# Performance work log

Hardware: AMD Instinct MI355X
Metric: run time of the kernel (lower is better)

Reference implementation:

```python
import jax, jax.numpy as jnp
import numpy as np

K_TAPS = 4

def setup_inputs() -> dict:
    key = jax.random.key(0)
    ks = jax.random.split(key, 7)
    B, T, E, N, F, H, K = 4, 64, 1, 512, 32, 64, K_TAPS
    stdv = 1.0 / np.sqrt(F * K)
    x  = jax.random.normal(ks[0], (B, T, F, N), jnp.float32)
    z0 = jax.random.normal(ks[1], (B, H, N), jnp.float32)
    # scale GSO so repeated S-products stay bounded
    S  = jax.random.normal(ks[2], (B, T, E, N, N), jnp.float32) / np.sqrt(N)
    aW = jax.random.uniform(ks[3], (H, E, K, F), jnp.float32, -stdv, stdv)
    bW = jax.random.uniform(ks[4], (H, E, K, H), jnp.float32, -stdv, stdv)
    xBias = jax.random.uniform(ks[5], (H, 1), jnp.float32, -stdv, stdv)
    zBias = jax.random.uniform(ks[6], (H, 1), jnp.float32, -stdv, stdv)
    return {"x": x, "z0": z0, "S": S, "aW": aW, "bW": bW,
            "xBias": xBias, "zBias": zBias}

def _lsigf_db(h, S, x, b):
    # h: (F_out,E,K,G), S: (B,T,E,N,N), x: (B,T,G,N)
    B, T, G, N = x.shape
    E = S.shape[2]
    K = h.shape[2]
    xk = jnp.broadcast_to(x[:, :, None], (B, T, E, G, N))
    zs = [xk]
    for _ in range(1, K):
        # delay one step, then shift with current-time GSO: x(t-k) S(t-k+1)...S(t)
        xk = jnp.concatenate([jnp.zeros_like(xk[:, :1]), xk[:, :-1]], axis=1)
        xk = jnp.einsum('btegm,btemn->btegn', xk, S)
        zs.append(xk)
    z = jnp.stack(zs, axis=2)                      # (B,T,K,E,G,N)
    y = jnp.einsum('fekg,btkegn->btfn', h, z)      # (B,T,F_out,N)
    if b is not None:
        y = y + b
    return y

def reference(x, z0, S, aW, bW, xBias, zBias):
    B, T, F, N = x.shape
    H, E, K, _ = bW.shape
    sigma = jnp.tanh
    Ax = _lsigf_db(aW, S, x, xBias)                # (B,T,H,N)
    # delayed hidden-state stack, zero padded to K taps; tap 0 holds z0
    Sz0 = jnp.zeros((B, K, E, H, N), x.dtype).at[:, 0].set(
        jnp.broadcast_to(z0[:, None], (B, E, H, N)))
    Bz0 = jnp.einsum('hekg,bkegn->bhn', bW, Sz0) + zBias
    zt0 = sigma(Ax[:, 0] + Bz0)

    def step(carry, inp):
        zt, Sz = carry                             # zt:(B,H,N) Sz:(B,K,E,H,N)
        Axt, St = inp                              # Axt:(B,H,N) St:(B,E,N,N)
        tail = jnp.einsum('bkehm,bemn->bkehn', Sz[:, :K - 1], St)
        head = jnp.broadcast_to(zt[:, None, None], (B, 1, E, H, N))
        Sz = jnp.concatenate([head, tail], axis=1)
        Bzt = jnp.einsum('hekg,bkegn->bhn', bW, Sz) + zBias
        zt = sigma(Axt + Bzt)
        return (zt, Sz), zt

    Ax_rest = jnp.moveaxis(Ax[:, 1:], 1, 0)        # (T-1,B,H,N)
    S_rest = jnp.moveaxis(S[:, 1:], 1, 0)          # (T-1,B,E,N,N)
    _, z_rest = jax.lax.scan(step, (zt0, Sz0), (Ax_rest, S_rest))
    z = jnp.concatenate([zt0[:, None], jnp.moveaxis(z_rest, 0, 1)], axis=1)
    return z                                       # (B,T,H,N)
```

## Files before the change

### kernel.cpp

```cpp
#include <hip/hip_runtime.h>
#include <math.h>

#define B_  4
#define T_  64
#define F_  32
#define N_  512
#define H_  64

#define CN     32
#define NCB    (N_/CN)
#define AROWS  288
#define JW     384
#define NWAVES 9
#define NTHR   (NWAVES*64)

typedef __attribute__((ext_vector_type(8))) short short8;
typedef __attribute__((ext_vector_type(4))) float float4_;
typedef unsigned short u16;
typedef unsigned int   u32;

__device__ __host__ inline u16 f2bf(float x) {
    union { float f; u32 u; } v; v.f = x;
    u32 r = v.u + 0x7fff + ((v.u >> 16) & 1);
    return (u16)(r >> 16);
}
__device__ inline float bf2f(u16 h) {
    union { float f; u32 u; } v; v.u = ((u32)h) << 16;
    return v.f;
}

__global__ void init_wc(const float* __restrict__ aW, const float* __restrict__ bW,
                        const float* __restrict__ xB, const float* __restrict__ zB,
                        u16* __restrict__ Wch, u16* __restrict__ Wcl,
                        float* __restrict__ bsum) {
    int idx = blockIdx.x * blockDim.x + threadIdx.x;
    if (idx < H_ * JW) {
        int h = idx / JW, j = idx % JW;
        float w;
        if (j < 96)       w = aW[(h*4 + (j>>5) + 1)*F_ + (j&31)];
        else if (j < 288) { int jj = j - 96; w = bW[(h*4 + (jj>>6) + 1)*H_ + (jj&63)]; }
        else if (j < 320) w = aW[(h*4)*F_ + (j - 288)];
        else              w = bW[(h*4)*H_ + (j - 320)];
        u16 hi = f2bf(w);
        Wch[idx] = hi;
        Wcl[idx] = f2bf(w - bf2f(hi));
    }
    if (idx < H_) bsum[idx] = xB[idx] + zB[idx];
}

__global__ __launch_bounds__(NTHR) void step_kernel(
    const float* __restrict__ x, const float* __restrict__ z0,
    const float* __restrict__ S,
    const u16* __restrict__ Wch, const u16* __restrict__ Wcl,
    const float* __restrict__ bsum, float* __restrict__ out,
    const u16* __restrict__ Aph, const u16* __restrict__ Apl,
    u16* __restrict__ Anh, u16* __restrict__ Anl,
    int t)
{
    __shared__ __align__(16) u16 Slds[2][2][CN][40];
    __shared__ __align__(16) u32 Clds[2][CN][196];

    const int tid  = threadIdx.x;
    const int wave = tid >> 6;
    const int lane = tid & 63;
    const int c16  = lane & 15;
    const int g4   = lane >> 4;

    const int b  = blockIdx.x & 3;
    const int cb = blockIdx.x >> 2;
    const int n0 = cb * CN;

    const float* Sbt = S + (size_t)(b*T_ + t) * N_ * N_;

    if (tid < 512) {
        const int col = tid & 31;
        const int rb  = (tid >> 5) * 6;
        #pragma unroll
        for (int j = 0; j < 6; ++j) {
            int row = rb + j;
            float v; int arow;
            if (row < 32) {
                v = x[((size_t)(b*T_ + t)*F_ + row) * N_ + n0 + col];
                arow = row;
            } else {
                int hz = row - 32;
                v = (t == 0)
                    ? z0[((size_t)b*H_ + hz) * N_ + n0 + col]
                    : out[((size_t)(b*T_ + (t-1))*H_ + hz) * N_ + n0 + col];
                arow = 96 + hz;
            }
            u16 hi = f2bf(v);
            u16 lo = f2bf(v - bf2f(hi));
            ((u16*)&Clds[0][col][0])[288 + row] = hi;
            ((u16*)&Clds[1][col][0])[288 + row] = lo;
            size_t ai = ((size_t)b*AROWS + arow) * N_ + n0 + col;
            Anh[ai] = hi; Anl[ai] = lo;
        }
    }

    if (t == 0) {
        for (int i = tid; i < CN*144; i += NTHR) {
            int n = i / 144, rp = i % 144;
            Clds[0][n][rp] = 0; Clds[1][n][rp] = 0;
        }
        for (int i = tid; i < 192*(CN/2); i += NTHR) {
            int r = i / (CN/2), c2 = i % (CN/2);
            int arow = (r < 64) ? 32 + r : 96 + r;
            size_t ai = ((size_t)b*AROWS + arow) * N_ + n0;
            ((u32*)(Anh + ai))[c2] = 0;
            ((u32*)(Anl + ai))[c2] = 0;
        }
    } else {
        const int r0 = wave * 32;
        const u16* Ah0 = Aph + ((size_t)b*AROWS + r0 + c16) * N_;
        const u16* Al0 = Apl + ((size_t)b*AROWS + r0 + c16) * N_;

        auto stage = [&](int ks, int buf) {
            if (tid < 512) {
                int col = tid & 31;
                int rbase = tid >> 5;
                #pragma unroll
                for (int hh = 0; hh < 2; ++hh) {
                    int row = rbase + 16*hh;
                    float v = Sbt[(size_t)(ks*32 + row) * N_ + n0 + col];
                    u16 hi = f2bf(v);
                    u16 lo = f2bf(v - bf2f(hi));
                    Slds[buf][0][col][row] = hi;
                    Slds[buf][1][col][row] = lo;
                }
            }
        };

        float4_ acc[2][2];
        #pragma unroll
        for (int i = 0; i < 2; ++i)
            #pragma unroll
            for (int j = 0; j < 2; ++j) acc[i][j] = (float4_){0.f,0.f,0.f,0.f};

        stage(0, 0);
        short8 ah[2], al[2];
        #pragma unroll
        for (int rf = 0; rf < 2; ++rf) {
            ah[rf] = *(const short8*)(Ah0 + (size_t)rf*16*N_ + g4*8);
            al[rf] = *(const short8*)(Al0 + (size_t)rf*16*N_ + g4*8);
        }
        __syncthreads();

        for (int ks = 0; ks < 16; ++ks) {
            const int buf = ks & 1;
            if (ks < 15) stage(ks + 1, buf ^ 1);
            short8 ahn[2], aln[2];
            if (ks < 15) {
                #pragma unroll
                for (int rf = 0; rf < 2; ++rf) {
                    ahn[rf] = *(const short8*)(Ah0 + (size_t)rf*16*N_ + (ks+1)*32 + g4*8);
                    aln[rf] = *(const short8*)(Al0 + (size_t)rf*16*N_ + (ks+1)*32 + g4*8);
                }
            }
            short8 bh[2], bl[2];
            #pragma unroll
            for (int nf = 0; nf < 2; ++nf) {
                bh[nf] = *(const short8*)&Slds[buf][0][nf*16 + c16][g4*8];
                bl[nf] = *(const short8*)&Slds[buf][1][nf*16 + c16][g4*8];
            }
            #pragma unroll
            for (int rf = 0; rf < 2; ++rf)
                #pragma unroll
                for (int nf = 0; nf < 2; ++nf) {
                    acc[rf][nf] = __builtin_amdgcn_mfma_f32_16x16x32_bf16(ah[rf], bh[nf], acc[rf][nf], 0,0,0);
                    acc[rf][nf] = __builtin_amdgcn_mfma_f32_16x16x32_bf16(ah[rf], bl[nf], acc[rf][nf], 0,0,0);
                    acc[rf][nf] = __builtin_amdgcn_mfma_f32_16x16x32_bf16(al[rf], bh[nf], acc[rf][nf], 0,0,0);
                }
            if (ks < 15) {
                ah[0]=ahn[0]; ah[1]=ahn[1]; al[0]=aln[0]; al[1]=aln[1];
            }
            __syncthreads();
        }

        const int aoff = (wave < 2) ? 32 : (wave >= 3 && wave <= 6) ? 64 : -1;
        #pragma unroll
        for (int rf = 0; rf < 2; ++rf) {
            int crow = r0 + rf*16 + g4*4;
            int rp   = crow >> 1;
            #pragma unroll
            for (int nf = 0; nf < 2; ++nf) {
                int n = nf*16 + c16;
                float4_ a = acc[rf][nf];
                u16 h0=f2bf(a.x), h1=f2bf(a.y), h2=f2bf(a.z), h3=f2bf(a.w);
                u16 l0=f2bf(a.x - bf2f(h0)), l1=f2bf(a.y - bf2f(h1));
                u16 l2=f2bf(a.z - bf2f(h2)), l3=f2bf(a.w - bf2f(h3));
                Clds[0][n][rp]   = (u32)h0 | ((u32)h1 << 16);
                Clds[0][n][rp+1] = (u32)h2 | ((u32)h3 << 16);
                Clds[1][n][rp]   = (u32)l0 | ((u32)l1 << 16);
                Clds[1][n][rp+1] = (u32)l2 | ((u32)l3 << 16);
                if (aoff > 0) {
                    size_t base = ((size_t)b*AROWS + crow + aoff) * N_ + n0 + n;
                    Anh[base]        = h0; Anl[base]        = l0;
                    Anh[base +   N_] = h1; Anl[base +   N_] = l1;
                    Anh[base + 2*N_] = h2; Anl[base + 2*N_] = l2;
                    Anh[base + 3*N_] = h3; Anl[base + 3*N_] = l3;
                }
            }
        }
    }
    __syncthreads();

    if (wave < 8) {
        const int hf = wave >> 1;
        const int nf = wave & 1;
        float4_ a2 = (float4_){0.f,0.f,0.f,0.f};
        const u16* Wh0 = Wch + (size_t)(hf*16 + c16) * JW;
        const u16* Wl0 = Wcl + (size_t)(hf*16 + c16) * JW;
        const u16* Th = (const u16*)&Clds[0][nf*16 + c16][0];
        const u16* Tl = (const u16*)&Clds[1][nf*16 + c16][0];
        #pragma unroll 4
        for (int kf = 0; kf < 12; ++kf) {
            short8 wh = *(const short8*)(Wh0 + kf*32 + g4*8);
            short8 wl = *(const short8*)(Wl0 + kf*32 + g4*8);
            short8 th = *(const short8*)(Th + kf*32 + g4*8);
            short8 tl = *(const short8*)(Tl + kf*32 + g4*8);
            a2 = __builtin_amdgcn_mfma_f32_16x16x32_bf16(wh, th, a2, 0,0,0);
            a2 = __builtin_amdgcn_mfma_f32_16x16x32_bf16(wh, tl, a2, 0,0,0);
            a2 = __builtin_amdgcn_mfma_f32_16x16x32_bf16(wl, th, a2, 0,0,0);
        }
        const int h0r = hf*16 + g4*4;
        const float4 bsv = *(const float4*)(bsum + h0r);
        float zx = tanhf(a2.x + bsv.x);
        float zy = tanhf(a2.y + bsv.y);
        float zz = tanhf(a2.z + bsv.z);
        float zw = tanhf(a2.w + bsv.w);
        size_t ob = ((size_t)(b*T_ + t)*H_ + h0r) * N_ + n0 + nf*16 + c16;
        out[ob]        = zx;
        out[ob +   N_] = zy;
        out[ob + 2*N_] = zz;
        out[ob + 3*N_] = zw;
    }
}

extern "C" void kernel_launch(void* const* d_in, const int* in_sizes, int n_in,
                              void* d_out, int out_size, void* d_ws, size_t ws_size,
                              hipStream_t stream) {
    const float* x  = (const float*)d_in[0];
    const float* z0 = (const float*)d_in[1];
    const float* S  = (const float*)d_in[2];
    const float* aW = (const float*)d_in[3];
    const float* bW = (const float*)d_in[4];
    const float* xB = (const float*)d_in[5];
    const float* zB = (const float*)d_in[6];
    float* out = (float*)d_out;

    char* p = (char*)d_ws;
    u16*   Wch  = (u16*)p;   p += (size_t)H_*JW*2;
    u16*   Wcl  = (u16*)p;   p += (size_t)H_*JW*2;
    float* bsum = (float*)p; p += 256;
    const size_t asz = (size_t)B_*AROWS*N_*2;
    u16* Ah[2]; u16* Al[2];
    Ah[0] = (u16*)p; p += asz;
    Al[0] = (u16*)p; p += asz;
    Ah[1] = (u16*)p; p += asz;
    Al[1] = (u16*)p; p += asz;

    init_wc<<<96, 256, 0, stream>>>(aW, bW, xB, zB, Wch, Wcl, bsum);
    for (int t = 0; t < T_; ++t) {
        const int pb = t & 1, nb = pb ^ 1;
        step_kernel<<<B_*NCB, NTHR, 0, stream>>>(x, z0, S, Wch, Wcl, bsum, out,
                                                 Ah[pb], Al[pb], Ah[nb], Al[nb], t);
    }
}
```

Measured before the change: 2.463 ms.

## Fuse all timesteps into one persistent cooperative kernel with grid sync

Replaces the 64 per-timestep kernel launches with a single cooperative kernel that loops over time and uses grid.sync between steps. It halves the column stripe width so the grid has twice as many blocks, and caches the combined weight matrix in LDS once per block. It also prefetches the first S tile of the next timestep during the last k-step of the current one. This removes per-launch overhead and repeated global weight loads. In exchange it depends on cooperative launch residency, uses much more LDS per block, and gives each wave less MFMA work per step.

```diff
diff --git a/kernel.cpp b/kernel.cpp
--- a/kernel.cpp
+++ b/kernel.cpp
@@ -1,5 +1,8 @@
 #include <hip/hip_runtime.h>
+#include <hip/hip_cooperative_groups.h>
 #include <math.h>
+
+namespace cg = cooperative_groups;
 
 #define B_  4
 #define T_  64
@@ -7,12 +10,13 @@
 #define N_  512
 #define H_  64
 
-#define CN     32
-#define NCB    (N_/CN)
-#define AROWS  288
-#define JW     384
-#define NWAVES 9
-#define NTHR   (NWAVES*64)
+#define CN      16
+#define NSTRIPE (N_/CN)
+#define NBLK    (B_*NSTRIPE)
+#define AROWS   288
+#define JW      384
+#define NWAVES  9
+#define NTHR    (NWAVES*64)
 
 typedef __attribute__((ext_vector_type(8))) short short8;
 typedef __attribute__((ext_vector_type(4))) float float4_;
@@ -48,17 +52,19 @@
     if (idx < H_) bsum[idx] = xB[idx] + zB[idx];
 }
 
-__global__ __launch_bounds__(NTHR) void step_kernel(
+__global__ __launch_bounds__(NTHR, 1) void run_all(
     const float* __restrict__ x, const float* __restrict__ z0,
     const float* __restrict__ S,
     const u16* __restrict__ Wch, const u16* __restrict__ Wcl,
     const float* __restrict__ bsum, float* __restrict__ out,
-    const u16* __restrict__ Aph, const u16* __restrict__ Apl,
-    u16* __restrict__ Anh, u16* __restrict__ Anl,
-    int t)
+    u16* __restrict__ A0h, u16* __restrict__ A0l,
+    u16* __restrict__ A1h, u16* __restrict__ A1l)
 {
-    __shared__ __align__(16) u16 Slds[2][2][CN][40];
-    __shared__ __align__(16) u32 Clds[2][CN][196];
+    cg::grid_group grid = cg::this_grid();
+
+    __shared__ __align__(16) u16 Sld[2][2][CN][40];
+    __shared__ __align__(16) u32 Cl[2][CN][196];
+    __shared__ __align__(16) u16 Wl[2][H_][JW + 8];
 
     const int tid  = threadIdx.x;
     const int wave = tid >> 6;
@@ -66,135 +72,134 @@
     const int c16  = lane & 15;
     const int g4   = lane >> 4;
 
-    const int b  = blockIdx.x & 3;
-    const int cb = blockIdx.x >> 2;
-    const int n0 = cb * CN;
-
-    const float* Sbt = S + (size_t)(b*T_ + t) * N_ * N_;
-
-    if (tid < 512) {
-        const int col = tid & 31;
-        const int rb  = (tid >> 5) * 6;
-        #pragma unroll
-        for (int j = 0; j < 6; ++j) {
-            int row = rb + j;
-            float v; int arow;
-            if (row < 32) {
-                v = x[((size_t)(b*T_ + t)*F_ + row) * N_ + n0 + col];
-                arow = row;
-            } else {
-                int hz = row - 32;
-                v = (t == 0)
-                    ? z0[((size_t)b*H_ + hz) * N_ + n0 + col]
-                    : out[((size_t)(b*T_ + (t-1))*H_ + hz) * N_ + n0 + col];
-                arow = 96 + hz;
-            }
+    const int blk    = blockIdx.x;
+    const int b      = (blk & 7) >> 1;
+    const int stripe = ((blk >> 3) << 1) | (blk & 1);
+    const int n0     = stripe * CN;
+    const int r0     = wave * 32;
+
+    for (int i = tid; i < H_ * JW; i += NTHR) {
+        int h = i / JW, j = i % JW;
+        Wl[0][h][j] = Wch[i];
+        Wl[1][h][j] = Wcl[i];
+    }
+
+    auto stageS = [&](int tt, int ks, int buf) {
+        if (tid < 512) {
+            int n = tid & 15;
+            int k = tid >> 4;
+            const float* Sp = S + (size_t)(b*T_ + tt) * N_ * N_;
+            float v = Sp[(size_t)(ks*32 + k) * N_ + n0 + n];
             u16 hi = f2bf(v);
-            u16 lo = f2bf(v - bf2f(hi));
-            ((u16*)&Clds[0][col][0])[288 + row] = hi;
-            ((u16*)&Clds[1][col][0])[288 + row] = lo;
-            size_t ai = ((size_t)b*AROWS + arow) * N_ + n0 + col;
-            Anh[ai] = hi; Anl[ai] = lo;
-        }
-    }
-
-    if (t == 0) {
-        for (int i = tid; i < CN*144; i += NTHR) {
-            int n = i / 144, rp = i % 144;
-            Clds[0][n][rp] = 0; Clds[1][n][rp] = 0;
-        }
-        for (int i = tid; i < 192*(CN/2); i += NTHR) {
-            int r = i / (CN/2), c2 = i % (CN/2);
-            int arow = (r < 64) ? 32 + r : 96 + r;
-            size_t ai = ((size_t)b*AROWS + arow) * N_ + n0;
-            ((u32*)(Anh + ai))[c2] = 0;
-            ((u32*)(Anl + ai))[c2] = 0;
-        }
-    } else {
-        const int r0 = wave * 32;
-        const u16* Ah0 = Aph + ((size_t)b*AROWS + r0 + c16) * N_;
-        const u16* Al0 = Apl + ((size_t)b*AROWS + r0 + c16) * N_;
-
-        auto stage = [&](int ks, int buf) {
+            Sld[buf][0][n][k] = hi;
+            Sld[buf][1][n][k] = f2bf(v - bf2f(hi));
+        }
+    };
+
+    for (int t = 0; t < T_; ++t) {
+        const int par = t & 1;
+        const u16* Aph = par ? A1h : A0h;
+        const u16* Apl = par ? A1l : A0l;
+        u16* Anh = par ? A0h : A1h;
+        u16* Anl = par ? A0l : A1l;
+
+        if (tid < 512) {
+            const int col = tid & 15;
+            const int rb  = (tid >> 4) * 3;
+            #pragma unroll
+            for (int j = 0; j < 3; ++j) {
+                int row = rb + j;
+                float v; int arow;
+                if (row < 32) {
+                    v = x[((size_t)(b*T_ + t)*F_ + row) * N_ + n0 + col];
+                    arow = row;
+                } else {
+                    int hz = row - 32;
+                    v = (t == 0)
+                        ? z0[((size_t)b*H_ + hz) * N_ + n0 + col]
+                        : out[((size_t)(b*T_ + (t-1))*H_ + hz) * N_ + n0 + col];
+                    arow = 96 + hz;
+                }
+                u16 hi = f2bf(v);
+                u16 lo = f2bf(v - bf2f(hi));
+                ((u16*)&Cl[0][col][0])[288 + row] = hi;
+                ((u16*)&Cl[1][col][0])[288 + row] = lo;
+                size_t ai = ((size_t)b*AROWS + arow) * N_ + n0 + col;
+                Anh[ai] = hi; Anl[ai] = lo;
+            }
+        }
+
+        if (t == 0) {
+            for (int i = tid; i < CN*144; i += NTHR) {
+                int n = i / 144, rp = i % 144;
+                Cl[0][n][rp] = 0; Cl[1][n][rp] = 0;
+            }
             if (tid < 512) {
-                int col = tid & 31;
-                int rbase = tid >> 5;
+                int col = tid & 15, rb = (tid >> 4) * 6;
                 #pragma unroll
-                for (int hh = 0; hh < 2; ++hh) {
-                    int row = rbase + 16*hh;
-                    float v = Sbt[(size_t)(ks*32 + row) * N_ + n0 + col];
-                    u16 hi = f2bf(v);
-                    u16 lo = f2bf(v - bf2f(hi));
-                    Slds[buf][0][col][row] = hi;
-                    Slds[buf][1][col][row] = lo;
-                }
-            }
-        };
-
-        float4_ acc[2][2];
-        #pragma unroll
-        for (int i = 0; i < 2; ++i)
+                for (int j = 0; j < 6; ++j) {
+                    int r = rb + j;
+                    int arow = (r < 64) ? 32 + r : 96 + r;
+                    size_t ai = ((size_t)b*AROWS + arow) * N_ + n0 + col;
+                    Anh[ai] = 0; Anl[ai] = 0;
+                }
+            }
+            stageS(1, 0, 0);
+        } else {
+            const u16* Ah0 = Aph + ((size_t)b*AROWS + r0 + c16) * N_;
+            const u16* Al0 = Apl + ((size_t)b*AROWS + r0 + c16) * N_;
+
+            float4_ acc[2];
+            acc[0] = (float4_){0.f,0.f,0.f,0.f};
+            acc[1] = (float4_){0.f,0.f,0.f,0.f};
+
+            short8 ah[2], al[2];
             #pragma unroll
-            for (int j = 0; j < 2; ++j) acc[i][j] = (float4_){0.f,0.f,0.f,0.f};
-
-        stage(0, 0);
-        short8 ah[2], al[2];
-        #pragma unroll
-        for (int rf = 0; rf < 2; ++rf) {
-            ah[rf] = *(const short8*)(Ah0 + (size_t)rf*16*N_ + g4*8);
-            al[rf] = *(const short8*)(Al0 + (size_t)rf*16*N_ + g4*8);
-        }
-        __syncthreads();
-
-        for (int ks = 0; ks < 16; ++ks) {
-            const int buf = ks & 1;
-            if (ks < 15) stage(ks + 1, buf ^ 1);
-            short8 ahn[2], aln[2];
-            if (ks < 15) {
+            for (int rf = 0; rf < 2; ++rf) {
+                ah[rf] = *(const short8*)(Ah0 + (size_t)rf*16*N_ + g4*8);
+                al[rf] = *(const short8*)(Al0 + (size_t)rf*16*N_ + g4*8);
+            }
+            __syncthreads();
+
+            for (int ks = 0; ks < 16; ++ks) {
+                const int buf = ks & 1;
+                if (ks < 15)          stageS(t, ks + 1, buf ^ 1);
+                else if (t < T_ - 1)  stageS(t + 1, 0, 0);
+                short8 ahn[2], aln[2];
+                if (ks < 15) {
+                    #pragma unroll
+                    for (int rf = 0; rf < 2; ++rf) {
+                        ahn[rf] = *(const short8*)(Ah0 + (size_t)rf*16*N_ + (ks+1)*32 + g4*8);
+                        aln[rf] = *(const short8*)(Al0 + (size_t)rf*16*N_ + (ks+1)*32 + g4*8);
+                    }
+                }
+                short8 bh = *(const short8*)&Sld[buf][0][c16][g4*8];
+                short8 bl = *(const short8*)&Sld[buf][1][c16][g4*8];
                 #pragma unroll
                 for (int rf = 0; rf < 2; ++rf) {
-                    ahn[rf] = *(const short8*)(Ah0 + (size_t)rf*16*N_ + (ks+1)*32 + g4*8);
-                    aln[rf] = *(const short8*)(Al0 + (size_t)rf*16*N_ + (ks+1)*32 + g4*8);
-                }
-            }
-            short8 bh[2], bl[2];
+                    acc[rf] = __builtin_amdgcn_mfma_f32_16x16x32_bf16(ah[rf], bh, acc[rf], 0,0,0);
+                    acc[rf] = __builtin_amdgcn_mfma_f32_16x16x32_bf16(ah[rf], bl, acc[rf], 0,0,0);
+                    acc[rf] = __builtin_amdgcn_mfma_f32_16x16x32_bf16(al[rf], bh, acc[rf], 0,0,0);
+                }
+                if (ks < 15) { ah[0]=ahn[0]; ah[1]=ahn[1]; al[0]=aln[0]; al[1]=aln[1]; }
+                __syncthreads();
+            }
+
+            const int aoff = (wave < 2) ? 32 : (wave >= 3 && wave <= 6) ? 64 : -1;
             #pragma unroll
-            for (int nf = 0; nf < 2; ++nf) {
-                bh[nf] = *(const short8*)&Slds[buf][0][nf*16 + c16][g4*8];
-                bl[nf] = *(const short8*)&Slds[buf][1][nf*16 + c16][g4*8];
-            }
-            #pragma unroll
-            for (int rf = 0; rf < 2; ++rf)
-                #pragma unroll
-                for (int nf = 0; nf < 2; ++nf) {
-                    acc[rf][nf] = __builtin_amdgcn_mfma_f32_16x16x32_bf16(ah[rf], bh[nf], acc[rf][nf], 0,0,0);
-                    acc[rf][nf] = __builtin_amdgcn_mfma_f32_16x16x32_bf16(ah[rf], bl[nf], acc[rf][nf], 0,0,0);
-                    acc[rf][nf] = __builtin_amdgcn_mfma_f32_16x16x32_bf16(al[rf], bh[nf], acc[rf][nf], 0,0,0);
-                }
-            if (ks < 15) {
-                ah[0]=ahn[0]; ah[1]=ahn[1]; al[0]=aln[0]; al[1]=aln[1];
-            }
-            __syncthreads();
-        }
-
-        const int aoff = (wave < 2) ? 32 : (wave >= 3 && wave <= 6) ? 64 : -1;
-        #pragma unroll
-        for (int rf = 0; rf < 2; ++rf) {
-            int crow = r0 + rf*16 + g4*4;
-            int rp   = crow >> 1;
-            #pragma unroll
-            for (int nf = 0; nf < 2; ++nf) {
-                int n = nf*16 + c16;
-                float4_ a = acc[rf][nf];
+            for (int rf = 0; rf < 2; ++rf) {
+                int crow = r0 + rf*16 + g4*4;
+                int rp   = crow >> 1;
+                float4_ a = acc[rf];
                 u16 h0=f2bf(a.x), h1=f2bf(a.y), h2=f2bf(a.z), h3=f2bf(a.w);
                 u16 l0=f2bf(a.x - bf2f(h0)), l1=f2bf(a.y - bf2f(h1));
                 u16 l2=f2bf(a.z - bf2f(h2)), l3=f2bf(a.w - bf2f(h3));
-                Clds[0][n][rp]   = (u32)h0 | ((u32)h1 << 16);
-                Clds[0][n][rp+1] = (u32)h2 | ((u32)h3 << 16);
-                Clds[1][n][rp]   = (u32)l0 | ((u32)l1 << 16);
-                Clds[1][n][rp+1] = (u32)l2 | ((u32)l3 << 16);
+                Cl[0][c16][rp]   = (u32)h0 | ((u32)h1 << 16);
+                Cl[0][c16][rp+1] = (u32)h2 | ((u32)h3 << 16);
+                Cl[1][c16][rp]   = (u32)l0 | ((u32)l1 << 16);
+                Cl[1][c16][rp+1] = (u32)l2 | ((u32)l3 << 16);
                 if (aoff > 0) {
-                    size_t base = ((size_t)b*AROWS + crow + aoff) * N_ + n0 + n;
+                    size_t base = ((size_t)b*AROWS + crow + aoff) * N_ + n0 + c16;
                     Anh[base]        = h0; Anl[base]        = l0;
                     Anh[base +   N_] = h1; Anl[base +   N_] = l1;
                     Anh[base + 2*N_] = h2; Anl[base + 2*N_] = l2;
@@ -202,38 +207,35 @@
                 }
             }
         }
-    }
-    __syncthreads();
-
-    if (wave < 8) {
-        const int hf = wave >> 1;
-        const int nf = wave & 1;
-        float4_ a2 = (float4_){0.f,0.f,0.f,0.f};
-        const u16* Wh0 = Wch + (size_t)(hf*16 + c16) * JW;
-        const u16* Wl0 = Wcl + (size_t)(hf*16 + c16) * JW;
-        const u16* Th = (const u16*)&Clds[0][nf*16 + c16][0];
-        const u16* Tl = (const u16*)&Clds[1][nf*16 + c16][0];
-        #pragma unroll 4
-        for (int kf = 0; kf < 12; ++kf) {
-            short8 wh = *(const short8*)(Wh0 + kf*32 + g4*8);
-            short8 wl = *(const short8*)(Wl0 + kf*32 + g4*8);
-            short8 th = *(const short8*)(Th + kf*32 + g4*8);
-            short8 tl = *(const short8*)(Tl + kf*32 + g4*8);
-            a2 = __builtin_amdgcn_mfma_f32_16x16x32_bf16(wh, th, a2, 0,0,0);
-            a2 = __builtin_amdgcn_mfma_f32_16x16x32_bf16(wh, tl, a2, 0,0,0);
-            a2 = __builtin_amdgcn_mfma_f32_16x16x32_bf16(wl, th, a2, 0,0,0);
-        }
-        const int h0r = hf*16 + g4*4;
-        const float4 bsv = *(const float4*)(bsum + h0r);
-        float zx = tanhf(a2.x + bsv.x);
-        float zy = tanhf(a2.y + bsv.y);
-        float zz = tanhf(a2.z + bsv.z);
-        float zw = tanhf(a2.w + bsv.w);
-        size_t ob = ((size_t)(b*T_ + t)*H_ + h0r) * N_ + n0 + nf*16 + c16;
-        out[ob]        = zx;
-        out[ob +   N_] = zy;
-        out[ob + 2*N_] = zz;
-        out[ob + 3*N_] = zw;
+        __syncthreads();
+
+        if (wave < 4) {
+            const int hf = wave;
+            float4_ a2 = (float4_){0.f,0.f,0.f,0.f};
+            const u16* Whp = &Wl[0][hf*16 + c16][0];
+            const u16* Wlp = &Wl[1][hf*16 + c16][0];
+            const u16* Th  = (const u16*)&Cl[0][c16][0];
+            const u16* Tl  = (const u16*)&Cl[1][c16][0];
+            #pragma unroll 4
+            for (int kf = 0; kf < 12; ++kf) {
+                short8 wh = *(const short8*)(Whp + kf*32 + g4*8);
+                short8 wl = *(const short8*)(Wlp + kf*32 + g4*8);
+                short8 th = *(const short8*)(Th  + kf*32 + g4*8);
+                short8 tl = *(const short8*)(Tl  + kf*32 + g4*8);
+                a2 = __builtin_amdgcn_mfma_f32_16x16x32_bf16(wh, th, a2, 0,0,0);
+                a2 = __builtin_amdgcn_mfma_f32_16x16x32_bf16(wh, tl, a2, 0,0,0);
+                a2 = __builtin_amdgcn_mfma_f32_16x16x32_bf16(wl, th, a2, 0,0,0);
+            }
+            const int h0r = hf*16 + g4*4;
+            const float4 bsv = *(const float4*)(bsum + h0r);
+            size_t ob = ((size_t)(b*T_ + t)*H_ + h0r) * N_ + n0 + c16;
+            out[ob]        = tanhf(a2.x + bsv.x);
+            out[ob +   N_] = tanhf(a2.y + bsv.y);
+            out[ob + 2*N_] = tanhf(a2.z + bsv.z);
+            out[ob + 3*N_] = tanhf(a2.w + bsv.w);
+        }
+
+        grid.sync();
     }
 }
 
@@ -254,16 +256,16 @@
     u16*   Wcl  = (u16*)p;   p += (size_t)H_*JW*2;
     float* bsum = (float*)p; p += 256;
     const size_t asz = (size_t)B_*AROWS*N_*2;
-    u16* Ah[2]; u16* Al[2];
-    Ah[0] = (u16*)p; p += asz;
-    Al[0] = (u16*)p; p += asz;
-    Ah[1] = (u16*)p; p += asz;
-    Al[1] = (u16*)p; p += asz;
+    u16* A0h = (u16*)p; p += asz;
+    u16* A0l = (u16*)p; p += asz;
+    u16* A1h = (u16*)p; p += asz;
+    u16* A1l = (u16*)p; p += asz;
 
     init_wc<<<96, 256, 0, stream>>>(aW, bW, xB, zB, Wch, Wcl, bsum);
-    for (int t = 0; t < T_; ++t) {
-        const int pb = t & 1, nb = pb ^ 1;
-        step_kernel<<<B_*NCB, NTHR, 0, stream>>>(x, z0, S, Wch, Wcl, bsum, out,
-                                                 Ah[pb], Al[pb], Ah[nb], Al[nb], t);
-    }
-}
+
+    void* args[] = { (void*)&x, (void*)&z0, (void*)&S, (void*)&Wch, (void*)&Wcl,
+                     (void*)&bsum, (void*)&out, (void*)&A0h, (void*)&A0l,
+                     (void*)&A1h, (void*)&A1l };
+    hipLaunchCooperativeKernel((void*)run_all, dim3(NBLK), dim3(NTHR),
+                               args, 0, stream);
+}
```

New measurement: 2.683 ms. 1.09x slower.
